# Kernel optimization log

Measured on AMD Instinct MI355X. Metric: run time of the kernel, lower is better.

Reference implementation:

```python
import jax, jax.numpy as jnp
import numpy as np

H_OUT, W_OUT = 48, 320


def setup_inputs() -> dict:
    key = jax.random.key(0)
    k1, k2, k3 = jax.random.split(key, 3)
    x = jax.random.normal(k1, (8, 64, 200, 320), dtype=jnp.float32)
    bboxes = jax.random.randint(k2, (256, 4), 0, 320, dtype=jnp.int32)
    box_img = jax.random.randint(k3, (256,), 0, 8, dtype=jnp.int32)
    return {"x": x, "bboxes": bboxes, "box_img": box_img}


def reference(x, bboxes, box_img):
    # x: [B, C, H, W]; bboxes: [N, 4] int (x0, y0, x1, y1); box_img: [N] image index
    B, C, H, W = x.shape
    x0 = jnp.clip(bboxes[:, 0], 0, W - 1)
    y0 = jnp.clip(bboxes[:, 1], 0, H - 1)
    x1 = jnp.clip(bboxes[:, 2], 0, W - 1)
    y1 = jnp.clip(bboxes[:, 3], 0, H - 1)
    x1 = jnp.maximum(x1, x0)
    y1 = jnp.maximum(y1, y0)
    # inclusive crop: height/width of each crop
    h = y1 - y0 + 1  # [N]
    w = x1 - x0 + 1  # [N]
    # F.interpolate default mode='nearest': src = floor(dst * in/out)
    i = jnp.arange(H_OUT, dtype=jnp.int32)
    j = jnp.arange(W_OUT, dtype=jnp.int32)
    rows = y0[:, None] + (i[None, :] * h[:, None]) // H_OUT  # [N, H_OUT]
    cols = x0[:, None] + (j[None, :] * w[:, None]) // W_OUT  # [N, W_OUT]
    # single fused gather: advanced indices broadcast to [N, H_OUT, W_OUT],
    # with the ':' channel slice moved to the last axis -> [N, H_OUT, W_OUT, C]
    g = x[box_img[:, None, None], :, rows[:, :, None], cols[:, None, :]]
    return jnp.transpose(g, (0, 3, 1, 2))  # [N, C, H_OUT, W_OUT]
```

## Files before the change

### kernel.cpp

```cpp
#include <hip/hip_runtime.h>

#define C_CH   64
#define H_IN   200
#define W_IN   320
#define H_OUT  48
#define W_OUT  320
#define N_BOX  256

typedef float float4v __attribute__((ext_vector_type(4), aligned(16)));

typedef __attribute__((address_space(3))) void       lds_vp;
typedef __attribute__((address_space(1))) const void gbl_vp;

__device__ __forceinline__ void glds16(const float* g, float* l) {
    __builtin_amdgcn_global_load_lds((gbl_vp*)g, (lds_vp*)l, 16, 0, 0);
}

__global__ __launch_bounds__(320) void roi_crop_kernel(
    const float* __restrict__ x,
    const int*   __restrict__ bboxes,
    const int*   __restrict__ box_img,
    float*       __restrict__ out)
{
    __shared__ __align__(16) float tile[H_OUT * 80 * 4];

    const int box = blockIdx.x;
    const int c   = blockIdx.y;
    const int t   = threadIdx.x;

    const int4 bb = *(const int4*)(bboxes + box * 4);
    int x0 = min(max(bb.x, 0), W_IN - 1);
    int y0 = min(max(bb.y, 0), H_IN - 1);
    int x1 = min(max(bb.z, 0), W_IN - 1);
    int y1 = min(max(bb.w, 0), H_IN - 1);
    x1 = max(x1, x0);
    y1 = max(y1, y0);

    const int h   = y1 - y0 + 1;
    const int w   = x1 - x0 + 1;
    const int img = box_img[box];

    const float* __restrict__ plane_in =
        x + ((size_t)img * C_CH + c) * (H_IN * W_IN);
    float* __restrict__ plane_out =
        out + ((size_t)box * C_CH + c) * (H_OUT * W_OUT);

    const int x0f4 = x0 >> 2;
    const int K4   = (x1 >> 2) - x0f4 + 1;
    const int x0f  = x0f4 << 2;
    const int nur  = (h < H_OUT) ? h : H_OUT;
    const bool small_h = (h <= H_OUT);

    for (int s = 0; s < nur; ++s) {
        const int rs = small_h ? (y0 + s) : (y0 + (s * h) / H_OUT);
        if (t < K4)
            glds16(plane_in + (size_t)rs * W_IN + x0f + (t << 2),
                   &tile[(s * K4 + t) << 2]);
    }
    __syncthreads();

    const int ldrow = K4 << 2;
    float4v* __restrict__ out4 = (float4v*)plane_out;
    #pragma unroll
    for (int k = 0; k < 12; ++k) {
        const int p = t + k * 320;
        const int i = p / 80;
        const int u = p - i * 80;
        const int s = small_h ? (i * h) / H_OUT : i;
        const int base = s * ldrow - x0f;
        float4v v;
        #pragma unroll
        for (int e = 0; e < 4; ++e) {
            const int ce = x0 + ((4 * u + e) * w) / W_OUT;
            v[e] = tile[base + ce];
        }
        out4[p] = v;
    }
}

extern "C" void kernel_launch(void* const* d_in, const int* in_sizes, int n_in,
                              void* d_out, int out_size, void* d_ws, size_t ws_size,
                              hipStream_t stream) {
    const float* x       = (const float*)d_in[0];
    const int*   bboxes  = (const int*)d_in[1];
    const int*   box_img = (const int*)d_in[2];
    float*       out     = (float*)d_out;

    dim3 grid(N_BOX, C_CH);
    dim3 block(320);
    roi_crop_kernel<<<grid, block, 0, stream>>>(x, bboxes, box_img, out);
}
```

Baseline: 1.114 ms.

## Split output rows into slices per block and load full input rows directly

Each block now handles a 12-row slice of one box/channel plane, which gives a grid four times larger with a much smaller LDS tile. Full 320-wide input rows are loaded with plain float4 global loads into registers and then stored to LDS, replacing the async global-to-LDS copies that fetched only the cropped span. Channels are now the fastest-varying grid dimension, so neighbouring blocks read the same image region across channels. The aim is higher occupancy and better load parallelism. The cost is reading whole rows (extra bytes when the crop is narrow) and re-reading duplicate rows when h is below 48.

After: 1.094 ms. About the same (-1.8%).

```diff
diff --git a/kernel.cpp b/kernel.cpp
--- a/kernel.cpp
+++ b/kernel.cpp
@@ -6,15 +6,10 @@
 #define H_OUT  48
 #define W_OUT  320
 #define N_BOX  256
+#define SLICE  12
+#define NSLICE (H_OUT / SLICE)
 
 typedef float float4v __attribute__((ext_vector_type(4), aligned(16)));
-
-typedef __attribute__((address_space(3))) void       lds_vp;
-typedef __attribute__((address_space(1))) const void gbl_vp;
-
-__device__ __forceinline__ void glds16(const float* g, float* l) {
-    __builtin_amdgcn_global_load_lds((gbl_vp*)g, (lds_vp*)l, 16, 0, 0);
-}
 
 __global__ __launch_bounds__(320) void roi_crop_kernel(
     const float* __restrict__ x,
@@ -22,10 +17,11 @@
     const int*   __restrict__ box_img,
     float*       __restrict__ out)
 {
-    __shared__ __align__(16) float tile[H_OUT * 80 * 4];
+    __shared__ __align__(16) float tile[SLICE * W_IN];
 
-    const int box = blockIdx.x;
-    const int c   = blockIdx.y;
+    const int c   = blockIdx.x;
+    const int box = blockIdx.y;
+    const int i0  = blockIdx.z * SLICE;
     const int t   = threadIdx.x;
 
     const int4 bb = *(const int4*)(bboxes + box * 4);
@@ -45,36 +41,33 @@
     float* __restrict__ plane_out =
         out + ((size_t)box * C_CH + c) * (H_OUT * W_OUT);
 
-    const int x0f4 = x0 >> 2;
-    const int K4   = (x1 >> 2) - x0f4 + 1;
-    const int x0f  = x0f4 << 2;
-    const int nur  = (h < H_OUT) ? h : H_OUT;
-    const bool small_h = (h <= H_OUT);
-
-    for (int s = 0; s < nur; ++s) {
-        const int rs = small_h ? (y0 + s) : (y0 + (s * h) / H_OUT);
-        if (t < K4)
-            glds16(plane_in + (size_t)rs * W_IN + x0f + (t << 2),
-                   &tile[(s * K4 + t) << 2]);
+    float4v v[3];
+    #pragma unroll
+    for (int k = 0; k < 3; ++k) {
+        const int p   = t + k * 320;
+        const int il  = p / 80;
+        const int wrd = p - il * 80;
+        const int r   = y0 + ((i0 + il) * h) / H_OUT;
+        v[k] = *(const float4v*)(plane_in + (size_t)r * W_IN + wrd * 4);
     }
+    #pragma unroll
+    for (int k = 0; k < 3; ++k)
+        *(float4v*)&tile[(t + k * 320) * 4] = v[k];
     __syncthreads();
 
-    const int ldrow = K4 << 2;
     float4v* __restrict__ out4 = (float4v*)plane_out;
     #pragma unroll
-    for (int k = 0; k < 12; ++k) {
-        const int p = t + k * 320;
-        const int i = p / 80;
-        const int u = p - i * 80;
-        const int s = small_h ? (i * h) / H_OUT : i;
-        const int base = s * ldrow - x0f;
-        float4v v;
+    for (int k = 0; k < 3; ++k) {
+        const int p  = t + k * 320;
+        const int il = p / 80;
+        const int u  = p - il * 80;
+        float4v o;
         #pragma unroll
         for (int e = 0; e < 4; ++e) {
             const int ce = x0 + ((4 * u + e) * w) / W_OUT;
-            v[e] = tile[base + ce];
+            o[e] = tile[il * W_IN + ce];
         }
-        out4[p] = v;
+        out4[(size_t)(i0 + il) * 80 + u] = o;
     }
 }
 
@@ -86,7 +79,7 @@
     const int*   box_img = (const int*)d_in[2];
     float*       out     = (float*)d_out;
 
-    dim3 grid(N_BOX, C_CH);
+    dim3 grid(C_CH, N_BOX, NSLICE);
     dim3 block(320);
     roi_crop_kernel<<<grid, block, 0, stream>>>(x, bboxes, box_img, out);
 }
```
